# Performance work log

Hardware: AMD Instinct MI355X
Metric: run time of the kernel (lower is better)

Reference implementation:

```python
import jax, jax.numpy as jnp
import numpy as np

STRIDE = 16.0
CROP_H = 14
CROP_W = 14


def setup_inputs() -> dict:
    key = jax.random.key(0)
    k1, k2, k3, k4, k5 = jax.random.split(key, 5)
    N, C, H, W = 4, 256, 50, 50
    M = 512
    feature_map = jax.random.normal(k1, (N, C, H, W), dtype=jnp.float32)
    # boxes in original-image coords (image ~800x800), x1<x2, y1<y2
    x1 = jax.random.uniform(k2, (M,), minval=0.0, maxval=600.0)
    y1 = jax.random.uniform(k3, (M,), minval=0.0, maxval=600.0)
    bw = jax.random.uniform(k4, (M, 2), minval=16.0, maxval=199.0)
    boxes = jnp.stack([x1, y1, x1 + bw[:, 0], y1 + bw[:, 1]], axis=1).astype(jnp.float32)
    box_idx = jax.random.randint(k5, (M,), 0, N, dtype=jnp.int32)
    return {"feature_map": feature_map, "boxes": boxes, "box_idx": box_idx}


def _roi_align(feature_map, boxes, box_idx):
    # TF-style crop_and_resize: sample a CROP_H x CROP_W bilinear grid per box,
    # zero extrapolation outside the feature map.
    H, W = feature_map.shape[2], feature_map.shape[3]
    b = boxes / STRIDE  # image coords -> feature-map coords
    x1, y1, x2, y2 = b[:, 0], b[:, 1], b[:, 2], b[:, 3]
    iy = jnp.arange(CROP_H, dtype=b.dtype)
    ix = jnp.arange(CROP_W, dtype=b.dtype)
    ys = y1[:, None] + iy[None, :] * (y2 - y1)[:, None] / (CROP_H - 1)  # (M, oH)
    xs = x1[:, None] + ix[None, :] * (x2 - x1)[:, None] / (CROP_W - 1)  # (M, oW)

    def crop_one(bi, ys_m, xs_m):
        fm = feature_map[bi]  # (C, H, W) -- gathered per box
        y0 = jnp.floor(ys_m)
        x0 = jnp.floor(xs_m)
        wy = (ys_m - y0)[None, :, None]            # (1, oH, 1)
        wx = (xs_m - x0)[None, None, :] if False else (xs_m - x0)  # (oW,)
        y0i = jnp.clip(y0.astype(jnp.int32), 0, H - 1)
        y1i = jnp.clip(y0i + 1, 0, H - 1)
        x0i = jnp.clip(x0.astype(jnp.int32), 0, W - 1)
        x1i = jnp.clip(x0i + 1, 0, W - 1)
        # interpolate along W first: (C, H, oW)
        g = fm[:, :, x0i] * (1.0 - wx) + fm[:, :, x1i] * wx
        # then along H: (C, oH, oW)
        out = g[:, y0i, :] * (1.0 - wy) + g[:, y1i, :] * wy
        valid = (((ys_m >= 0) & (ys_m <= H - 1))[:, None]
                 & ((xs_m >= 0) & (xs_m <= W - 1))[None, :])
        return jnp.where(valid[None, :, :], out, 0.0)

    return jax.vmap(crop_one)(box_idx, ys, xs)  # (M, C, oH, oW)


def reference(feature_map, boxes, box_idx):
    return _roi_align(feature_map, boxes, box_idx)
```

## Files before the change

### kernel.cpp

```cpp
#include <hip/hip_runtime.h>


typedef float f32x4 __attribute__((ext_vector_type(4)));

constexpr int C_DIM = 256;
constexpr int H_DIM = 50;
constexpr int W_DIM = 50;
constexpr int M_BOX = 512;
constexpr int CW    = 14;
constexpr int NPOS  = 196;
constexpr int CCH   = 16;
constexpr int PLANE  = H_DIM * W_DIM;
constexpr int WC  = 16;
constexpr int WSZ = 256;
constexpr float INV_STRIDE = 1.0f / 16.0f;

__global__ __launch_bounds__(256) void roi_align_v11(
    const float* __restrict__ fm,
    const float* __restrict__ boxes,
    const int*   __restrict__ box_idx,
    float*       __restrict__ out)
{
    __shared__ float Wnd[CCH * WSZ];

    int bid   = blockIdx.x;
    int xcd   = bid & 7;
    int w     = bid >> 3;
    int m     = w >> 1;
    int cbase = xcd * 32 + (w & 1) * CCH;

    int t  = threadIdx.x;
    int wv = t >> 6;
    int l  = t & 63;

    float4 bx = reinterpret_cast<const float4*>(boxes)[m];
    int bi = box_idx[m];
    float x1 = bx.x * INV_STRIDE;
    float y1 = bx.y * INV_STRIDE;
    float x2 = bx.z * INV_STRIDE;
    float y2 = bx.w * INV_STRIDE;

    int xLo = min(max((int)floorf(x1), 0), W_DIM - 1);
    int yLo = min(max((int)floorf(y1), 0), H_DIM - 1);
    int xW  = min(xLo, W_DIM - WC);

    {
        int row  = l >> 2;
        int quad = l & 3;
        int gy   = min(yLo + row, H_DIM - 1);
        const float* g0 = fm + ((size_t)(bi * C_DIM + cbase + wv * 4)) * PLANE
                             + gy * W_DIM + xW + quad * 4;
        #pragma unroll
        for (int k = 0; k < 4; ++k) {
            const float* g  = g0 + (size_t)k * PLANE;
            float*       l0 = &Wnd[(wv * 4 + k) * WSZ];
            __builtin_amdgcn_global_load_lds(
                (const __attribute__((address_space(1))) unsigned int*)g,
                (__attribute__((address_space(3))) unsigned int*)l0,
                16, 0, 0);
        }
    }

    if (l < 49) {
        int q = l;

        int   w00[4];
        float wxv[4], owx[4], wyv[4], owy[4];
        #pragma unroll
        for (int e = 0; e < 4; ++e) {
            int p  = 4 * q + e;
            int iy = p / CW;
            int ix = p - iy * CW;
            float ys = y1 + ((float)iy * (y2 - y1)) / 13.0f;
            float xs = x1 + ((float)ix * (x2 - x1)) / 13.0f;
            float y0f = floorf(ys);
            float x0f = floorf(xs);
            float wy = ys - y0f;
            float wx = xs - x0f;
            int y0i = min(max((int)y0f, 0), H_DIM - 1);
            int x0i = min(max((int)x0f, 0), W_DIM - 1);
            bool vld = (ys >= 0.0f) && (ys <= (float)(H_DIM - 1)) &&
                       (xs >= 0.0f) && (xs <= (float)(W_DIM - 1));
            w00[e] = (y0i - yLo) * WC + (x0i - xW);
            wxv[e] = vld ? wx : 0.0f;
            owx[e] = vld ? (1.0f - wx) : 0.0f;
            wyv[e] = wy; owy[e] = 1.0f - wy;
        }

        asm volatile("s_waitcnt vmcnt(0)" ::: "memory");

        const float* wp = &Wnd[(size_t)(wv * 4) * WSZ];
        float* op = out + ((size_t)m * C_DIM + cbase + wv * 4) * NPOS + 4 * q;

        #pragma unroll
        for (int k = 0; k < 4; ++k) {
            float rv[4];
            #pragma unroll
            for (int e = 0; e < 4; ++e) {
                float f00 = wp[w00[e]];
                float f01 = wp[w00[e] + 1];
                float f10 = wp[w00[e] + WC];
                float f11 = wp[w00[e] + WC + 1];
                float top = f00 * owx[e] + f01 * wxv[e];
                float bot = f10 * owx[e] + f11 * wxv[e];
                rv[e] = top * owy[e] + bot * wyv[e];
            }
            f32x4 r;
            r.x = rv[0]; r.y = rv[1]; r.z = rv[2]; r.w = rv[3];
            __builtin_nontemporal_store(r, reinterpret_cast<f32x4*>(op));
            wp += WSZ;
            op += NPOS;
        }
    }
}

extern "C" void kernel_launch(void* const* d_in, const int* in_sizes, int n_in,
                              void* d_out, int out_size, void* d_ws, size_t ws_size,
                              hipStream_t stream) {
    const float* fm      = (const float*)d_in[0];
    const float* boxes   = (const float*)d_in[1];
    const int*   box_idx = (const int*)d_in[2];
    float* out = (float*)d_out;

    dim3 block(256);
    dim3 grid(M_BOX * (C_DIM / CCH) );
    hipLaunchKernelGGL(roi_align_v11, grid, block, 0, stream,
                       fm, boxes, box_idx, out);
}
```

Baseline: 29.95 us.

## Double-buffer LDS window staging across channel groups and two boxes per block

Blocks drop from 8192 to 2048. Each block now handles two boxes times 32 channels, in eight items of 8 channels each. Global-to-LDS window loads go into two alternating buffers, so the next item's load overlaps the current item's bilinear compute and stores, with vmcnt waits counted by hand. The aim is to hide load latency and cut per-block launch overhead and box setup, at the cost of fragile wait counting and fewer resident blocks.

Result: slower. 35.69 us (+19.1%).

```diff
diff --git a/kernel.cpp b/kernel.cpp
--- a/kernel.cpp
+++ b/kernel.cpp
@@ -9,108 +9,143 @@
 constexpr int M_BOX = 512;
 constexpr int CW    = 14;
 constexpr int NPOS  = 196;
-constexpr int CCH   = 16;
-constexpr int PLANE  = H_DIM * W_DIM;
-constexpr int WC  = 16;
-constexpr int WSZ = 256;
+constexpr int PLANE = H_DIM * W_DIM;
+constexpr int WC    = 16;
+constexpr int WSZ   = 256;
+constexpr int ITEM_CH = 8;
 constexpr float INV_STRIDE = 1.0f / 16.0f;
 
-__global__ __launch_bounds__(256) void roi_align_v11(
+struct SC { int bi, yLo, xW; float x1, y1, x2, y2; };
+struct WT { int w00[4]; float wx[4], ox[4], wy[4], oy[4]; };
+
+__device__ __forceinline__ SC mk_sc(const float* boxes, const int* bidx, int m) {
+    float4 bx = reinterpret_cast<const float4*>(boxes)[m];
+    SC s;
+    s.bi = bidx[m];
+    s.x1 = bx.x * INV_STRIDE; s.y1 = bx.y * INV_STRIDE;
+    s.x2 = bx.z * INV_STRIDE; s.y2 = bx.w * INV_STRIDE;
+    int xLo = min(max((int)floorf(s.x1), 0), W_DIM - 1);
+    s.yLo = min(max((int)floorf(s.y1), 0), H_DIM - 1);
+    s.xW  = min(xLo, W_DIM - WC);
+    return s;
+}
+
+__device__ __forceinline__ void mk_wt(const SC& s, int q, WT& W) {
+    #pragma unroll
+    for (int e = 0; e < 4; ++e) {
+        int p  = 4 * q + e;
+        int iy = p / CW;
+        int ix = p - iy * CW;
+        float ys = s.y1 + ((float)iy * (s.y2 - s.y1)) / 13.0f;
+        float xs = s.x1 + ((float)ix * (s.x2 - s.x1)) / 13.0f;
+        float y0f = floorf(ys);
+        float x0f = floorf(xs);
+        float wy = ys - y0f;
+        float wx = xs - x0f;
+        int y0i = min(max((int)y0f, 0), H_DIM - 1);
+        int x0i = min(max((int)x0f, 0), W_DIM - 1);
+        bool v = (ys >= 0.0f) && (ys <= (float)(H_DIM - 1)) &&
+                 (xs >= 0.0f) && (xs <= (float)(W_DIM - 1));
+        W.w00[e] = (y0i - s.yLo) * WC + (x0i - s.xW);
+        W.wx[e] = v ? wx : 0.0f;
+        W.ox[e] = v ? (1.0f - wx) : 0.0f;
+        W.wy[e] = wy; W.oy[e] = 1.0f - wy;
+    }
+}
+
+__device__ __forceinline__ void stage(const float* fm, const SC& s, int cb,
+                                      int wv, int l, float* buf) {
+    int row  = l >> 2;
+    int quad = l & 3;
+    int gy   = min(s.yLo + row, H_DIM - 1);
+    const float* g0 = fm + ((size_t)(s.bi * C_DIM + cb + wv * 2)) * PLANE
+                         + gy * W_DIM + s.xW + quad * 4;
+    float* l0 = &buf[(wv * 2) * WSZ];
+    __builtin_amdgcn_global_load_lds(
+        (const __attribute__((address_space(1))) unsigned int*)g0,
+        (__attribute__((address_space(3))) unsigned int*)l0, 16, 0, 0);
+    __builtin_amdgcn_global_load_lds(
+        (const __attribute__((address_space(1))) unsigned int*)(g0 + PLANE),
+        (__attribute__((address_space(3))) unsigned int*)(l0 + WSZ), 16, 0, 0);
+}
+
+__device__ __forceinline__ void comp(const float* buf, const WT& W, float* out,
+                                     int m, int cb, int wv, int q) {
+    const float* wp = &buf[(wv * 2) * WSZ];
+    float* op = out + ((size_t)m * C_DIM + cb + wv * 2) * NPOS + 4 * q;
+    #pragma unroll
+    for (int k = 0; k < 2; ++k) {
+        float rv[4];
+        #pragma unroll
+        for (int e = 0; e < 4; ++e) {
+            float f00 = wp[W.w00[e]];
+            float f01 = wp[W.w00[e] + 1];
+            float f10 = wp[W.w00[e] + WC];
+            float f11 = wp[W.w00[e] + WC + 1];
+            float top = f00 * W.ox[e] + f01 * W.wx[e];
+            float bot = f10 * W.ox[e] + f11 * W.wx[e];
+            rv[e] = top * W.oy[e] + bot * W.wy[e];
+        }
+        f32x4 r;
+        r.x = rv[0]; r.y = rv[1]; r.z = rv[2]; r.w = rv[3];
+        __builtin_nontemporal_store(r, reinterpret_cast<f32x4*>(op));
+        wp += WSZ;
+        op += NPOS;
+    }
+}
+
+__global__ __launch_bounds__(256, 8) void roi_align_v13(
     const float* __restrict__ fm,
     const float* __restrict__ boxes,
     const int*   __restrict__ box_idx,
     float*       __restrict__ out)
 {
-    __shared__ float Wnd[CCH * WSZ];
+    __shared__ float B0[ITEM_CH * WSZ];
+    __shared__ float B1[ITEM_CH * WSZ];
 
-    int bid   = blockIdx.x;
-    int xcd   = bid & 7;
-    int w     = bid >> 3;
-    int m     = w >> 1;
-    int cbase = xcd * 32 + (w & 1) * CCH;
+    int bid  = blockIdx.x;
+    int xcd  = bid & 7;
+    int bxl  = bid >> 3;
+    int cb_x = xcd * 32;
+    int m0   = 2 * bxl;
+    int m1   = m0 + 1;
 
     int t  = threadIdx.x;
     int wv = t >> 6;
     int l  = t & 63;
+    int q  = l;
+    int qq = min(l, 48);
 
-    float4 bx = reinterpret_cast<const float4*>(boxes)[m];
-    int bi = box_idx[m];
-    float x1 = bx.x * INV_STRIDE;
-    float y1 = bx.y * INV_STRIDE;
-    float x2 = bx.z * INV_STRIDE;
-    float y2 = bx.w * INV_STRIDE;
+    SC s0 = mk_sc(boxes, box_idx, m0);
+    SC s1;
+    WT W;
+    mk_wt(s0, qq, W);
 
-    int xLo = min(max((int)floorf(x1), 0), W_DIM - 1);
-    int yLo = min(max((int)floorf(y1), 0), H_DIM - 1);
-    int xW  = min(xLo, W_DIM - WC);
+    stage(fm, s0, cb_x + 0, wv, l, B0);
 
-    {
-        int row  = l >> 2;
-        int quad = l & 3;
-        int gy   = min(yLo + row, H_DIM - 1);
-        const float* g0 = fm + ((size_t)(bi * C_DIM + cbase + wv * 4)) * PLANE
-                             + gy * W_DIM + xW + quad * 4;
-        #pragma unroll
-        for (int k = 0; k < 4; ++k) {
-            const float* g  = g0 + (size_t)k * PLANE;
-            float*       l0 = &Wnd[(wv * 4 + k) * WSZ];
-            __builtin_amdgcn_global_load_lds(
-                (const __attribute__((address_space(1))) unsigned int*)g,
-                (__attribute__((address_space(3))) unsigned int*)l0,
-                16, 0, 0);
-        }
-    }
+    #pragma unroll
+    for (int j = 0; j < 8; ++j) {
+        float* bc = (j & 1) ? B1 : B0;
+        float* bn = (j & 1) ? B0 : B1;
+        int mcur  = (j < 4) ? m0 : m1;
+        int cb    = cb_x + (j & 3) * ITEM_CH;
 
-    if (l < 49) {
-        int q = l;
+        if (j == 3) s1 = mk_sc(boxes, box_idx, m1);
 
-        int   w00[4];
-        float wxv[4], owx[4], wyv[4], owy[4];
-        #pragma unroll
-        for (int e = 0; e < 4; ++e) {
-            int p  = 4 * q + e;
-            int iy = p / CW;
-            int ix = p - iy * CW;
-            float ys = y1 + ((float)iy * (y2 - y1)) / 13.0f;
-            float xs = x1 + ((float)ix * (x2 - x1)) / 13.0f;
-            float y0f = floorf(ys);
-            float x0f = floorf(xs);
-            float wy = ys - y0f;
-            float wx = xs - x0f;
-            int y0i = min(max((int)y0f, 0), H_DIM - 1);
-            int x0i = min(max((int)x0f, 0), W_DIM - 1);
-            bool vld = (ys >= 0.0f) && (ys <= (float)(H_DIM - 1)) &&
-                       (xs >= 0.0f) && (xs <= (float)(W_DIM - 1));
-            w00[e] = (y0i - yLo) * WC + (x0i - xW);
-            wxv[e] = vld ? wx : 0.0f;
-            owx[e] = vld ? (1.0f - wx) : 0.0f;
-            wyv[e] = wy; owy[e] = 1.0f - wy;
+        if (j < 7) {
+            int jn = j + 1;
+            stage(fm, (jn < 4) ? s0 : s1, cb_x + (jn & 3) * ITEM_CH, wv, l, bn);
         }
 
-        asm volatile("s_waitcnt vmcnt(0)" ::: "memory");
+        if (j == 4) mk_wt(s1, qq, W);
 
-        const float* wp = &Wnd[(size_t)(wv * 4) * WSZ];
-        float* op = out + ((size_t)m * C_DIM + cbase + wv * 4) * NPOS + 4 * q;
+        if (j == 0 || j == 7) {
+            asm volatile("s_waitcnt vmcnt(2)" ::: "memory");
+        } else {
+            asm volatile("s_waitcnt vmcnt(4)" ::: "memory");
+        }
 
-        #pragma unroll
-        for (int k = 0; k < 4; ++k) {
-            float rv[4];
-            #pragma unroll
-            for (int e = 0; e < 4; ++e) {
-                float f00 = wp[w00[e]];
-                float f01 = wp[w00[e] + 1];
-                float f10 = wp[w00[e] + WC];
-                float f11 = wp[w00[e] + WC + 1];
-                float top = f00 * owx[e] + f01 * wxv[e];
-                float bot = f10 * owx[e] + f11 * wxv[e];
-                rv[e] = top * owy[e] + bot * wyv[e];
-            }
-            f32x4 r;
-            r.x = rv[0]; r.y = rv[1]; r.z = rv[2]; r.w = rv[3];
-            __builtin_nontemporal_store(r, reinterpret_cast<f32x4*>(op));
-            wp += WSZ;
-            op += NPOS;
-        }
+        if (l < 49) comp(bc, W, out, mcur, cb, wv, q);
     }
 }
 
@@ -123,7 +158,7 @@
     float* out = (float*)d_out;
 
     dim3 block(256);
-    dim3 grid(M_BOX * (C_DIM / CCH) );
-    hipLaunchKernelGGL(roi_align_v11, grid, block, 0, stream,
+    dim3 grid(2048);
+    hipLaunchKernelGGL(roi_align_v13, grid, block, 0, stream,
                        fm, boxes, box_idx, out);
 }
```

## Process two channel groups per block with overlapped LDS window loads

Applied to the files above, without the earlier changes.

Each block now handles 32 channels in two 16-channel halves with separate LDS windows, issuing all window loads up front and computing the first half while the second half's loads are still in flight, using partial vmcnt waits. The grid is halved accordingly. The per-sample coordinate math now multiplies by a precomputed 1/13 instead of dividing. This doubles LDS per block, which may lower occupancy, and the reciprocal can change rounding slightly.

Result: slower. 31.70 us (+5.8%).

```diff
diff --git a/kernel.cpp b/kernel.cpp
--- a/kernel.cpp
+++ b/kernel.cpp
@@ -14,20 +14,22 @@
 constexpr int WC  = 16;
 constexpr int WSZ = 256;
 constexpr float INV_STRIDE = 1.0f / 16.0f;
+constexpr float INV13 = 1.0f / 13.0f;
 
-__global__ __launch_bounds__(256) void roi_align_v11(
+__global__ __launch_bounds__(256) void roi_align_v16(
     const float* __restrict__ fm,
     const float* __restrict__ boxes,
     const int*   __restrict__ box_idx,
     float*       __restrict__ out)
 {
-    __shared__ float Wnd[CCH * WSZ];
+    __shared__ float WA[CCH * WSZ];
+    __shared__ float WB[CCH * WSZ];
 
-    int bid   = blockIdx.x;
-    int xcd   = bid & 7;
-    int w     = bid >> 3;
-    int m     = w >> 1;
-    int cbase = xcd * 32 + (w & 1) * CCH;
+    int bid = blockIdx.x;
+    int xcd = bid & 7;
+    int m   = bid >> 3;
+    int cb0 = xcd * 32;
+    int cb1 = cb0 + CCH;
 
     int t  = threadIdx.x;
     int wv = t >> 6;
@@ -48,31 +50,40 @@
         int row  = l >> 2;
         int quad = l & 3;
         int gy   = min(yLo + row, H_DIM - 1);
-        const float* g0 = fm + ((size_t)(bi * C_DIM + cbase + wv * 4)) * PLANE
+        const float* gA = fm + ((size_t)(bi * C_DIM + cb0 + wv * 4)) * PLANE
+                             + gy * W_DIM + xW + quad * 4;
+        const float* gB = fm + ((size_t)(bi * C_DIM + cb1 + wv * 4)) * PLANE
                              + gy * W_DIM + xW + quad * 4;
         #pragma unroll
         for (int k = 0; k < 4; ++k) {
-            const float* g  = g0 + (size_t)k * PLANE;
-            float*       l0 = &Wnd[(wv * 4 + k) * WSZ];
             __builtin_amdgcn_global_load_lds(
-                (const __attribute__((address_space(1))) unsigned int*)g,
-                (__attribute__((address_space(3))) unsigned int*)l0,
+                (const __attribute__((address_space(1))) unsigned int*)(gA + (size_t)k * PLANE),
+                (__attribute__((address_space(3))) unsigned int*)&WA[(wv * 4 + k) * WSZ],
+                16, 0, 0);
+        }
+        #pragma unroll
+        for (int k = 0; k < 4; ++k) {
+            __builtin_amdgcn_global_load_lds(
+                (const __attribute__((address_space(1))) unsigned int*)(gB + (size_t)k * PLANE),
+                (__attribute__((address_space(3))) unsigned int*)&WB[(wv * 4 + k) * WSZ],
                 16, 0, 0);
         }
     }
 
+    int   w00[4];
+    float wxv[4], owx[4], wyv[4], owy[4];
+    float* opA;
     if (l < 49) {
         int q = l;
-
-        int   w00[4];
-        float wxv[4], owx[4], wyv[4], owy[4];
+        float sy = (y2 - y1) * INV13;
+        float sx = (x2 - x1) * INV13;
         #pragma unroll
         for (int e = 0; e < 4; ++e) {
             int p  = 4 * q + e;
             int iy = p / CW;
             int ix = p - iy * CW;
-            float ys = y1 + ((float)iy * (y2 - y1)) / 13.0f;
-            float xs = x1 + ((float)ix * (x2 - x1)) / 13.0f;
+            float ys = y1 + (float)iy * sy;
+            float xs = x1 + (float)ix * sx;
             float y0f = floorf(ys);
             float x0f = floorf(xs);
             float wy = ys - y0f;
@@ -86,12 +97,38 @@
             owx[e] = vld ? (1.0f - wx) : 0.0f;
             wyv[e] = wy; owy[e] = 1.0f - wy;
         }
+        opA = out + ((size_t)m * C_DIM + cb0 + wv * 4) * NPOS + 4 * q;
+    }
 
-        asm volatile("s_waitcnt vmcnt(0)" ::: "memory");
+    asm volatile("s_waitcnt vmcnt(4)" ::: "memory");
+    if (l < 49) {
+        const float* wp = &WA[(size_t)(wv * 4) * WSZ];
+        float* op = opA;
+        #pragma unroll
+        for (int k = 0; k < 4; ++k) {
+            float rv[4];
+            #pragma unroll
+            for (int e = 0; e < 4; ++e) {
+                float f00 = wp[w00[e]];
+                float f01 = wp[w00[e] + 1];
+                float f10 = wp[w00[e] + WC];
+                float f11 = wp[w00[e] + WC + 1];
+                float top = f00 * owx[e] + f01 * wxv[e];
+                float bot = f10 * owx[e] + f11 * wxv[e];
+                rv[e] = top * owy[e] + bot * wyv[e];
+            }
+            f32x4 r;
+            r.x = rv[0]; r.y = rv[1]; r.z = rv[2]; r.w = rv[3];
+            __builtin_nontemporal_store(r, reinterpret_cast<f32x4*>(op));
+            wp += WSZ;
+            op += NPOS;
+        }
+    }
 
-        const float* wp = &Wnd[(size_t)(wv * 4) * WSZ];
-        float* op = out + ((size_t)m * C_DIM + cbase + wv * 4) * NPOS + 4 * q;
-
+    asm volatile("s_waitcnt vmcnt(4)" ::: "memory");
+    if (l < 49) {
+        const float* wp = &WB[(size_t)(wv * 4) * WSZ];
+        float* op = opA + (size_t)CCH * NPOS;
         #pragma unroll
         for (int k = 0; k < 4; ++k) {
             float rv[4];
@@ -123,7 +160,7 @@
     float* out = (float*)d_out;
 
     dim3 block(256);
-    dim3 grid(M_BOX * (C_DIM / CCH) );
-    hipLaunchKernelGGL(roi_align_v11, grid, block, 0, stream,
+    dim3 grid(M_BOX * 8);
+    hipLaunchKernelGGL(roi_align_v16, grid, block, 0, stream,
                        fm, boxes, box_idx, out);
 }
```
